# Kernel tuning notes

Measured on AMD Instinct MI355X. Metric: run time of the kernel, lower is better.

The kernel has to match this reference:

```python
import jax, jax.numpy as jnp
import numpy as np

N_GROUPS, K_POS, HID, M_NEG = 4096, 4, 256, 256


def setup_inputs() -> dict:
    key = jax.random.key(0)
    k1, k2, k3 = jax.random.split(key, 3)
    n, k, h, m = N_GROUPS, K_POS, HID, M_NEG
    embeddings = jax.random.normal(k1, (n * k, h), dtype=jnp.float32)
    # linear_predictor: Linear((k-1)*h -> h)
    W = jax.random.normal(k2, (h, (k - 1) * h), dtype=jnp.float32) / np.float32(np.sqrt((k - 1) * h))
    b = jnp.zeros((h,), dtype=jnp.float32)
    # grouped targets: k consecutive samples share a class id
    target = (jnp.arange(n * k, dtype=jnp.int32) // k).astype(jnp.int32)
    # column index into each group's sorted list of (n-1)*k negatives
    neg_perm = jax.random.randint(k3, (n, m), 0, (n - 1) * k, dtype=jnp.int32)
    return {
        "embeddings": embeddings,
        "W": W,
        "b": b,
        "target": target,
        "neg_perm": neg_perm,
        "k_pos_samples": K_POS,
    }


def reference(embeddings, W, b, target, neg_perm, k_pos_samples):
    # target is implicit in the contiguous group layout (k identical ids per group)
    N, h = embeddings.shape
    k = k_pos_samples
    n = N // k
    m = neg_perm.shape[1]

    e = embeddings.reshape(n, k, h)
    hist_x = e[:, : k - 1, :].reshape(n, (k - 1) * h)   # context: first k-1 of group
    hist_y = e[:, k - 1, :]                              # positive: last of group

    predicts = hist_x @ W.T + b                          # [n, h]
    pos_logit = jnp.sum(predicts * hist_y, axis=-1)      # [n]

    # sorted negatives for group i are {0..i*k-1} u {(i+1)*k..n*k-1};
    # candidate position j maps to global index j (j < i*k) else j + k
    row_off = jnp.arange(n, dtype=neg_perm.dtype)[:, None] * k
    neg_idx = neg_perm + jnp.where(neg_perm >= row_off, k, 0)  # [n, m]

    neg_embed = embeddings[neg_idx]                      # [n, m, h] big gather
    neg_logit = jnp.einsum('nh,nmh->nm', predicts, neg_embed)

    logits = jnp.concatenate([pos_logit[:, None], neg_logit], axis=-1)  # [n, 1+m]
    loss = -jnp.mean(jax.nn.log_softmax(logits, axis=-1)[:, 0])
    return loss
```

## Files before the change

### kernel.cpp

```cpp
#include <hip/hip_runtime.h>

#define N_GROUPS 4096
#define K_POS 4
#define HID 256
#define M_NEG 256
#define KDIM 768
#define N_EMB (N_GROUPS * K_POS)

typedef __attribute__((ext_vector_type(4))) float f32x4;
typedef __attribute__((ext_vector_type(4))) int i32x4;

#define QSCALE 32.0f
#define WSCALE 512.0f
#define QDESCALE (1.0f / (QSCALE * QSCALE))
#define GDESCALE (1.0f / (QSCALE * WSCALE))

__device__ inline int q8(float x, float scale) {
  int q = __float2int_rn(x * scale);
  return max(-127, min(127, q));
}
__device__ inline int pack4(float a, float b, float c, float d, float s) {
  return (q8(a, s) & 0xff) | ((q8(b, s) & 0xff) << 8) |
         ((q8(c, s) & 0xff) << 16) | ((q8(d, s) & 0xff) << 24);
}
__device__ inline int sb(int v, int k) { return (v << (24 - 8 * k)) >> 24; }

#define N4_EMB (N_EMB * HID / 4)
#define N4_W   (KDIM * HID / 4)
__global__ __launch_bounds__(256) void convert_in(
    const float* __restrict__ emb, const float* __restrict__ W,
    int* __restrict__ embQ, int* __restrict__ WQ) {
  const int i = blockIdx.x * 256 + threadIdx.x;
  if (i < N4_EMB) {
    const float4 v = ((const float4*)emb)[i];
    embQ[i] = pack4(v.x, v.y, v.z, v.w, QSCALE);
  } else if (i < N4_EMB + N4_W) {
    const int j = i - N4_EMB;
    const float4 v = ((const float4*)W)[j];
    WQ[j] = pack4(v.x, v.y, v.z, v.w, WSCALE);
  }
}

__global__ __launch_bounds__(256) void gemm_i8(
    const int* __restrict__ embQ, const int* __restrict__ WQ,
    const float* __restrict__ bias, int* __restrict__ predQ) {
  const int wv = threadIdx.x >> 6, l = threadIdx.x & 63;
  const int mt = blockIdx.x * 4 + wv;
  const int nt0 = blockIdx.y * 4;
  const int r = l & 15, g = l >> 4;
  __shared__ float sT[4][16 * 16];

  const int* A = embQ + (size_t)(mt * 16 + r) * (K_POS * HID / 4) + g * 4;
  i32x4 a[12];
#pragma unroll
  for (int kk = 0; kk < 12; ++kk) a[kk] = *(const i32x4*)(A + kk * 16);

#pragma unroll
  for (int j = 0; j < 4; ++j) {
    const int nt = nt0 + j;
    const int* B = WQ + (size_t)(nt * 16 + r) * (KDIM / 4) + g * 4;
    i32x4 acc = {0, 0, 0, 0};
#pragma unroll
    for (int kk = 0; kk < 12; ++kk) {
      const i32x4 b = *(const i32x4*)(B + kk * 16);
      acc = __builtin_amdgcn_mfma_i32_16x16x64_i8(a[kk], b, acc, 0, 0, 0);
    }
    const float bb = bias[nt * 16 + r];
#pragma unroll
    for (int i = 0; i < 4; ++i)
      sT[wv][(g * 4 + i) * 16 + r] = (float)acc[i] * GDESCALE + bb;
    const int row = l >> 2, cb = l & 3;
    const float4 v = *(const float4*)&sT[wv][row * 16 + cb * 4];
    predQ[(size_t)(mt * 16 + row) * (HID / 4) + nt * 4 + cb] =
        pack4(v.x, v.y, v.z, v.w, QSCALE);
  }
}

__global__ __launch_bounds__(256) void loss_mfma(
    const int* __restrict__ embQ, const int* __restrict__ predQ,
    const int* __restrict__ neg_perm, float* __restrict__ row_loss) {
  const int tid = threadIdx.x;
  const int lane = tid & 63, wv = tid >> 6;
  const int n = blockIdx.x * 2 + (wv >> 1);
  const int half = wv & 1;
  const int jl = lane & 15, g = lane >> 4;
  const int base = n * K_POS;
  __shared__ float smax[4], ssum[4], spos[4];

  const int* pq = predQ + (size_t)n * 64;
  i32x4 aQ[4];
#pragma unroll
  for (int kk = 0; kk < 4; ++kk) aQ[kk] = *(const i32x4*)(pq + kk * 16 + g * 4);

  float posv = 0.f;
  if (half == 0) {
    const int va = pq[lane];
    const int vb = embQ[(size_t)(base + K_POS - 1) * 64 + lane];
    int d = sb(va, 0) * sb(vb, 0) + sb(va, 1) * sb(vb, 1) +
            sb(va, 2) * sb(vb, 2) + sb(va, 3) * sb(vb, 3);
    float s = (float)d;
    s += __shfl_xor(s, 1);  s += __shfl_xor(s, 2);  s += __shfl_xor(s, 4);
    s += __shfl_xor(s, 8);  s += __shfl_xor(s, 16); s += __shfl_xor(s, 32);
    posv = s * QDESCALE;
  }

  const int* nb = neg_perm + (size_t)n * M_NEG + half * 128;
  int idx[8];
#pragma unroll
  for (int jt = 0; jt < 8; ++jt) {
    const int j = nb[jt * 16 + jl];
    idx[jt] = j + (j >= base ? K_POS : 0);
  }

  float m0 = -INFINITY, s0 = 0.f, m1 = -INFINITY, s1 = 0.f;
#pragma unroll
  for (int t = 0; t < 8; t += 2) {
    const int* bp0 = embQ + (size_t)idx[t] * 64 + g * 4;
    const int* bp1 = embQ + (size_t)idx[t + 1] * 64 + g * 4;
    i32x4 acc0 = {0, 0, 0, 0}, acc1 = {0, 0, 0, 0};
#pragma unroll
    for (int kk = 0; kk < 4; ++kk) {
      const i32x4 b0 = *(const i32x4*)(bp0 + kk * 16);
      acc0 = __builtin_amdgcn_mfma_i32_16x16x64_i8(aQ[kk], b0, acc0, 0, 0, 0);
    }
#pragma unroll
    for (int kk = 0; kk < 4; ++kk) {
      const i32x4 b1 = *(const i32x4*)(bp1 + kk * 16);
      acc1 = __builtin_amdgcn_mfma_i32_16x16x64_i8(aQ[kk], b1, acc1, 0, 0, 0);
    }
    const float v0 = (float)acc0[0] * QDESCALE;
    const float v1 = (float)acc1[0] * QDESCALE;
    { const float mn = fmaxf(m0, v0); s0 = s0 * __expf(m0 - mn) + __expf(v0 - mn); m0 = mn; }
    { const float mn = fmaxf(m1, v1); s1 = s1 * __expf(m1 - mn) + __expf(v1 - mn); m1 = mn; }
  }

  float m = fmaxf(m0, m1);
  float s = s0 * __expf(m0 - m) + s1 * __expf(m1 - m);

  float gm = m;
  gm = fmaxf(gm, __shfl_xor(gm, 1));  gm = fmaxf(gm, __shfl_xor(gm, 2));
  gm = fmaxf(gm, __shfl_xor(gm, 4));  gm = fmaxf(gm, __shfl_xor(gm, 8));
  gm = fmaxf(gm, __shfl_xor(gm, 16)); gm = fmaxf(gm, __shfl_xor(gm, 32));
  float sr = s * __expf(m - gm);
  sr += __shfl_xor(sr, 1);  sr += __shfl_xor(sr, 2);  sr += __shfl_xor(sr, 4);
  sr += __shfl_xor(sr, 8);  sr += __shfl_xor(sr, 16); sr += __shfl_xor(sr, 32);
  sr *= 0.25f;

  if (lane == 0) { smax[wv] = gm; ssum[wv] = sr; spos[wv] = posv; }
  __syncthreads();

  if (half == 0 && lane == 0) {
    const float ma = smax[wv], mb = smax[wv + 1];
    const float sa = ssum[wv], sb2 = ssum[wv + 1];
    const float pv = spos[wv];
    const float mm = fmaxf(fmaxf(ma, mb), pv);
    const float tot = sa * __expf(ma - mm) + sb2 * __expf(mb - mm) + __expf(pv - mm);
    row_loss[n] = __logf(tot) + mm - pv;
  }
}

__global__ __launch_bounds__(1024) void reduce_mean(
    const float* __restrict__ row_loss, float* __restrict__ out) {
  const int tid = threadIdx.x;
  const int lane = tid & 63, wv = tid >> 6;
  const float4 v = ((const float4*)row_loss)[tid];
  float s = v.x + v.y + v.z + v.w;
  s += __shfl_xor(s, 1);  s += __shfl_xor(s, 2);  s += __shfl_xor(s, 4);
  s += __shfl_xor(s, 8);  s += __shfl_xor(s, 16); s += __shfl_xor(s, 32);
  __shared__ float red[16];
  if (lane == 0) red[wv] = s;
  __syncthreads();
  if (tid == 0) {
    float t = 0.f;
#pragma unroll
    for (int i = 0; i < 16; ++i) t += red[i];
    out[0] = t * (1.0f / N_GROUPS);
  }
}

extern "C" void kernel_launch(void* const* d_in, const int* in_sizes, int n_in,
                              void* d_out, int out_size, void* d_ws, size_t ws_size,
                              hipStream_t stream) {
  const float* emb = (const float*)d_in[0];
  const float* W = (const float*)d_in[1];
  const float* b = (const float*)d_in[2];
  const int* neg_perm = (const int*)d_in[4];
  float* out = (float*)d_out;

  int* embQ = (int*)d_ws;
  int* WQ = embQ + (size_t)N_EMB * HID / 4;
  int* predQ = WQ + (size_t)KDIM * HID / 4;
  float* row_loss = (float*)(predQ + (size_t)N_GROUPS * HID / 4);

  const int n4 = N4_EMB + N4_W;
  convert_in<<<(n4 + 255) / 256, 256, 0, stream>>>(emb, W, embQ, WQ);
  gemm_i8<<<dim3(N_GROUPS / 64, 4), 256, 0, stream>>>(embQ, WQ, b, predQ);
  loss_mfma<<<N_GROUPS / 2, 256, 0, stream>>>(embQ, predQ, neg_perm, row_loss);
  reduce_mean<<<1, 1024, 0, stream>>>(row_loss, out);
}
```

Before: 55.32 us.

## Fuse embedding int8 quantization into the predictor GEMM kernel

Embedding quantization moves out of the standalone convert kernel and into the GEMM. Each GEMM block reads fp32 embeddings and packs them to int8 in registers, and the blockIdx.y==0 blocks also write the quantized rows, including the fourth positive row, for the loss kernel. This removes the extra pass that wrote embQ and then read it back. In exchange, all four y-blocks now read and quantize the fp32 context rows redundantly, which is four times more fp32 traffic for that part.

```diff
diff --git a/kernel.cpp b/kernel.cpp
--- a/kernel.cpp
+++ b/kernel.cpp
@@ -23,37 +23,58 @@
   return (q8(a, s) & 0xff) | ((q8(b, s) & 0xff) << 8) |
          ((q8(c, s) & 0xff) << 16) | ((q8(d, s) & 0xff) << 24);
 }
+__device__ inline int pack4v(const float4 v, float s) {
+  return pack4(v.x, v.y, v.z, v.w, s);
+}
 __device__ inline int sb(int v, int k) { return (v << (24 - 8 * k)) >> 24; }
 
-#define N4_EMB (N_EMB * HID / 4)
-#define N4_W   (KDIM * HID / 4)
-__global__ __launch_bounds__(256) void convert_in(
-    const float* __restrict__ emb, const float* __restrict__ W,
-    int* __restrict__ embQ, int* __restrict__ WQ) {
+#define N4_W (KDIM * HID / 4)
+__global__ __launch_bounds__(256) void convert_w(
+    const float* __restrict__ W, int* __restrict__ WQ) {
   const int i = blockIdx.x * 256 + threadIdx.x;
-  if (i < N4_EMB) {
-    const float4 v = ((const float4*)emb)[i];
-    embQ[i] = pack4(v.x, v.y, v.z, v.w, QSCALE);
-  } else if (i < N4_EMB + N4_W) {
-    const int j = i - N4_EMB;
-    const float4 v = ((const float4*)W)[j];
-    WQ[j] = pack4(v.x, v.y, v.z, v.w, WSCALE);
-  }
-}
-
-__global__ __launch_bounds__(256) void gemm_i8(
-    const int* __restrict__ embQ, const int* __restrict__ WQ,
-    const float* __restrict__ bias, int* __restrict__ predQ) {
+  const float4 v = ((const float4*)W)[i];
+  WQ[i] = pack4v(v, WSCALE);
+}
+
+__global__ __launch_bounds__(256) void gemm_fused(
+    const float* __restrict__ emb, const int* __restrict__ WQ,
+    const float* __restrict__ bias, int* __restrict__ embQ,
+    int* __restrict__ predQ) {
   const int wv = threadIdx.x >> 6, l = threadIdx.x & 63;
   const int mt = blockIdx.x * 4 + wv;
   const int nt0 = blockIdx.y * 4;
   const int r = l & 15, g = l >> 4;
   __shared__ float sT[4][16 * 16];
 
-  const int* A = embQ + (size_t)(mt * 16 + r) * (K_POS * HID / 4) + g * 4;
+  const int m = mt * 16 + r;
+  const float* Af = emb + (size_t)m * (K_POS * HID) + g * 16;
   i32x4 a[12];
 #pragma unroll
-  for (int kk = 0; kk < 12; ++kk) a[kk] = *(const i32x4*)(A + kk * 16);
+  for (int kk = 0; kk < 12; ++kk) {
+    const float4 f0 = *(const float4*)(Af + kk * 64);
+    const float4 f1 = *(const float4*)(Af + kk * 64 + 4);
+    const float4 f2 = *(const float4*)(Af + kk * 64 + 8);
+    const float4 f3 = *(const float4*)(Af + kk * 64 + 12);
+    i32x4 p = {pack4v(f0, QSCALE), pack4v(f1, QSCALE), pack4v(f2, QSCALE), pack4v(f3, QSCALE)};
+    a[kk] = p;
+  }
+
+  if (blockIdx.y == 0) {
+#pragma unroll
+    for (int kk = 0; kk < 12; ++kk)
+      *(i32x4*)(embQ + (size_t)m * 256 + kk * 16 + g * 4) = a[kk];
+    const int row = blockIdx.x * 64 + (threadIdx.x >> 2);
+    const int part = threadIdx.x & 3;
+#pragma unroll
+    for (int u = 0; u < 4; ++u) {
+      const float* tf = emb + (size_t)row * (K_POS * HID) + KDIM + part * 64 + u * 16;
+      i32x4 tq = {pack4v(*(const float4*)(tf), QSCALE),
+                  pack4v(*(const float4*)(tf + 4), QSCALE),
+                  pack4v(*(const float4*)(tf + 8), QSCALE),
+                  pack4v(*(const float4*)(tf + 12), QSCALE)};
+      *(i32x4*)(embQ + (size_t)row * 256 + 192 + part * 16 + u * 4) = tq;
+    }
+  }
 
 #pragma unroll
   for (int j = 0; j < 4; ++j) {
@@ -72,7 +93,7 @@
     const int row = l >> 2, cb = l & 3;
     const float4 v = *(const float4*)&sT[wv][row * 16 + cb * 4];
     predQ[(size_t)(mt * 16 + row) * (HID / 4) + nt * 4 + cb] =
-        pack4(v.x, v.y, v.z, v.w, QSCALE);
+        pack4v(v, QSCALE);
   }
 }
 
@@ -192,9 +213,8 @@
   int* predQ = WQ + (size_t)KDIM * HID / 4;
   float* row_loss = (float*)(predQ + (size_t)N_GROUPS * HID / 4);
 
-  const int n4 = N4_EMB + N4_W;
-  convert_in<<<(n4 + 255) / 256, 256, 0, stream>>>(emb, W, embQ, WQ);
-  gemm_i8<<<dim3(N_GROUPS / 64, 4), 256, 0, stream>>>(embQ, WQ, b, predQ);
+  convert_w<<<N4_W / 256, 256, 0, stream>>>(W, WQ);
+  gemm_fused<<<dim3(N_GROUPS / 64, 4), 256, 0, stream>>>(emb, WQ, b, embQ, predQ);
   loss_mfma<<<N_GROUPS / 2, 256, 0, stream>>>(embQ, predQ, neg_perm, row_loss);
   reduce_mean<<<1, 1024, 0, stream>>>(row_loss, out);
 }
```

Result: slower. 62.58 us (+13.1%).
